# Kernel tuning notes

Hardware: AMD Instinct MI355X
Metric: run time of the kernel (lower is better)

## Reference

```python
import jax, jax.numpy as jnp
from jax import lax
import numpy as np

F_IN, F_OUT, T = 32, 64, 8
H1 = (3 * F_IN + F_OUT) // 4  # 40
H2 = F_OUT                    # 64
N, E = 50000, 800000


def setup_inputs() -> dict:
    key = jax.random.key(0)
    ks = jax.random.split(key, 8)
    def p(k, shape, fan_in):
        return jax.random.normal(k, shape, jnp.float32) / np.float32(np.sqrt(fan_in))
    return {
        "temporal_features": jax.random.normal(ks[0], (N, F_IN, T), jnp.float32),
        "src": jax.random.randint(ks[1], (E,), 0, N, jnp.int32),
        "dst": jax.random.randint(ks[2], (E,), 0, N, jnp.int32),
        "W1": p(ks[3], (F_IN, H1), F_IN), "b1": jnp.zeros((H1,), jnp.float32),
        "W2": p(ks[4], (H1, H2), H1),   "b2": jnp.zeros((H2,), jnp.float32),
        "W3": p(ks[5], (H2, F_OUT), H2), "b3": jnp.zeros((F_OUT,), jnp.float32),
        "Wc": p(ks[6], (F_OUT, F_OUT, 3), F_OUT * 3),  # Conv1d weight [out, in, k]
        "bc": jnp.zeros((F_OUT,), jnp.float32),
    }


def _graph_conv(h, src, dst, out_norm, in_norm, W, b, act, n):
    # dgl GraphConv, norm='both': D_out^{-1/2} -> sum-aggregate -> D_in^{-1/2} -> linear
    h = h * out_norm[:, None, None]                       # [N, t, f]
    agg = jax.ops.segment_sum(h[src], dst, num_segments=n)  # irregular gather/scatter
    h = agg * in_norm[:, None, None]
    h = jnp.einsum("nti,io->nto", h, W) + b
    return jax.nn.relu(h) if act else h


def reference(temporal_features, src, dst, W1, b1, W2, b2, W3, b3, Wc, bc):
    n = temporal_features.shape[0]
    ones = jnp.ones(src.shape, temporal_features.dtype)
    out_deg = jax.ops.segment_sum(ones, src, num_segments=n)
    in_deg = jax.ops.segment_sum(ones, dst, num_segments=n)
    out_norm = jnp.clip(out_deg, 1.0, None) ** -0.5
    in_norm = jnp.clip(in_deg, 1.0, None) ** -0.5

    h = jnp.swapaxes(temporal_features, -2, -1)  # [N, t, f_in]
    h = _graph_conv(h, src, dst, out_norm, in_norm, W1, b1, True, n)
    h = _graph_conv(h, src, dst, out_norm, in_norm, W2, b2, True, n)
    h = _graph_conv(h, src, dst, out_norm, in_norm, W3, b3, False, n)
    h = jnp.swapaxes(h, -2, -1)  # [N, f_out, t]

    out = lax.conv_general_dilated(
        h, Wc, window_strides=(1,), padding=((1, 1),),
        dimension_numbers=("NCH", "OIH", "NCH"))
    return out + bc[None, :, None]
```

## Files before the change

kernel.cpp:

```cpp
#include <hip/hip_runtime.h>

typedef float f32x4 __attribute__((ext_vector_type(4)));


__global__ __launch_bounds__(256) void deg_kernel(const int* __restrict__ src,
                                                  const int* __restrict__ dst,
                                                  int* __restrict__ out_deg,
                                                  int* __restrict__ in_deg, int E) {
  int e = blockIdx.x * 256 + threadIdx.x;
  if (e < E) {
    atomicAdd(&out_deg[src[e]], 1);
    atomicAdd(&in_deg[dst[e]], 1);
  }
}

__global__ __launch_bounds__(256) void norm_kernel(const int* __restrict__ out_deg,
                                                   const int* __restrict__ in_deg,
                                                   float* __restrict__ out_norm,
                                                   float* __restrict__ in_norm, int N) {
  int n = blockIdx.x * 256 + threadIdx.x;
  if (n < N) {
    out_norm[n] = 1.0f / sqrtf((float)max(out_deg[n], 1));
    in_norm[n]  = 1.0f / sqrtf((float)max(in_deg[n], 1));
  }
}

__global__ __launch_bounds__(256) void wct_kernel(const float* __restrict__ Wc,
                                                  float* __restrict__ wct) {
  int m = blockIdx.x * 256 + threadIdx.x;
  if (m < 12288) wct[m] = Wc[(m & 63) * 192 + (m >> 6)];
}


__global__ __launch_bounds__(256) void scan_partial_kernel(const int* __restrict__ deg,
                                                           int* __restrict__ partial, int N) {
  __shared__ int ws[4];
  int tid = threadIdx.x, lane = tid & 63, wv = tid >> 6;
  int base = blockIdx.x * 1024;
  int v = 0;
#pragma unroll
  for (int k = 0; k < 4; ++k) {
    int i = base + tid + k * 256;
    if (i < N) v += deg[i];
  }
  for (int d = 32; d > 0; d >>= 1) v += __shfl_down(v, d, 64);
  if (lane == 0) ws[wv] = v;
  __syncthreads();
  if (tid == 0) partial[blockIdx.x] = ws[0] + ws[1] + ws[2] + ws[3];
}

__global__ __launch_bounds__(1024) void scan_partials_kernel(int* __restrict__ partial, int P) {
  __shared__ int wsum[16];
  int tid = threadIdx.x, lane = tid & 63, wv = tid >> 6;
  int v = (tid < P) ? partial[tid] : 0;
  int x = v;
  for (int d = 1; d < 64; d <<= 1) {
    int y = __shfl_up(x, d, 64);
    if (lane >= d) x += y;
  }
  if (lane == 63) wsum[wv] = x;
  __syncthreads();
  if (wv == 0 && lane < 16) {
    int y = wsum[lane];
    int z = y;
    for (int d = 1; d < 16; d <<= 1) {
      int q = __shfl_up(z, d, 64);
      if (lane >= d) z += q;
    }
    wsum[lane] = z - y;
  }
  __syncthreads();
  if (tid < P) partial[tid] = wsum[wv] + x - v;
}

__global__ __launch_bounds__(1024) void scan_apply_kernel(const int* __restrict__ deg,
                                                          const int* __restrict__ partial,
                                                          int* __restrict__ off, int N) {
  __shared__ int wsum[16];
  int tid = threadIdx.x, lane = tid & 63, wv = tid >> 6;
  int i = blockIdx.x * 1024 + tid;
  int v = (i < N) ? deg[i] : 0;
  int x = v;
  for (int d = 1; d < 64; d <<= 1) {
    int y = __shfl_up(x, d, 64);
    if (lane >= d) x += y;
  }
  if (lane == 63) wsum[wv] = x;
  __syncthreads();
  if (wv == 0 && lane < 16) {
    int y = wsum[lane];
    int z = y;
    for (int d = 1; d < 16; d <<= 1) {
      int q = __shfl_up(z, d, 64);
      if (lane >= d) z += q;
    }
    wsum[lane] = z - y;
  }
  __syncthreads();
  int excl = partial[blockIdx.x] + wsum[wv] + (x - v);
  if (i < N) off[i] = excl;
  if (i == N - 1) off[N] = excl + v;
}

__global__ __launch_bounds__(256) void scatter_kernel(const int* __restrict__ src,
                                                      const int* __restrict__ dst,
                                                      const int* __restrict__ in_off,
                                                      int* __restrict__ cursor,
                                                      int* __restrict__ csr_src, int E) {
  int e = blockIdx.x * 256 + threadIdx.x;
  if (e < E) {
    int d = dst[e];
    int p = atomicAdd(&cursor[d], 1);
    csr_src[in_off[d] + p] = src[e];
  }
}

template <int NC>
__device__ __forceinline__ void keepalive(f32x4* v) {
#pragma unroll
  for (int k = 0; k < NC; ++k) asm volatile("" : "+v"(v[k]));
}

template <int F_IN, int F_OUT, int TS, int L, bool IT_LAYOUT, bool RELU,
          bool GNORM, bool SCALE_OUT>
__device__ __forceinline__ void layer_body(
    const float* __restrict__ h_in, const int* __restrict__ csr_src,
    const int* __restrict__ in_off, const float* __restrict__ out_norm,
    const float* __restrict__ in_norm, const float* __restrict__ W,
    const float* __restrict__ bias, float* __restrict__ h_out, int N) {
  constexpr int NF4 = F_IN * 2;
  constexpr int NC = NF4 / L;
  constexpr int M = 64 / L;
  constexpr int SLOTS = 4 * M;
  constexpr int SLOT = (IT_LAYOUT ? F_IN * 8 : TS * 8) + 8;
  __shared__ float agg[SLOTS][SLOT];
  int tid = threadIdx.x;
  int wave = tid >> 6, lane = tid & 63;
  int q = lane / L, r = lane % L;
  int slot = wave * M + q;
  int n = blockIdx.x * SLOTS + slot;
  bool valid = (n < N);

  f32x4 acc[NC];
#pragma unroll
  for (int k = 0; k < NC; ++k) acc[k] = (f32x4){0.f, 0.f, 0.f, 0.f};

  if (valid) {
    int e0 = in_off[n], e1 = in_off[n + 1];
    const f32x4* h4 = (const f32x4*)h_in;
    int j = e0;
    if (e1 - e0 >= 2) {
      int sA = csr_src[j], sB = csr_src[j + 1];
      do {
        int cA = sA, cB = sB;
        int jn = j + 2;
        sA = csr_src[min(jn, e1 - 1)];
        sB = csr_src[min(jn + 1, e1 - 1)];
        float wA = 1.f, wB = 1.f;
        if constexpr (GNORM) { wA = out_norm[cA]; wB = out_norm[cB]; }
        const f32x4* pA = h4 + (size_t)cA * NF4 + r;
        const f32x4* pB = h4 + (size_t)cB * NF4 + r;
        f32x4 vA[NC], vB[NC];
#pragma unroll
        for (int k = 0; k < NC; ++k) vA[k] = pA[k * L];
#pragma unroll
        for (int k = 0; k < NC; ++k) vB[k] = pB[k * L];
        keepalive<NC>(vA);
        keepalive<NC>(vB);
#pragma unroll
        for (int k = 0; k < NC; ++k)
#pragma unroll
          for (int e = 0; e < 4; ++e) acc[k][e] = fmaf(vA[k][e], wA, acc[k][e]);
#pragma unroll
        for (int k = 0; k < NC; ++k)
#pragma unroll
          for (int e = 0; e < 4; ++e) acc[k][e] = fmaf(vB[k][e], wB, acc[k][e]);
        j = jn;
      } while (j + 2 <= e1);
    }
    if (j < e1) {
      int s = csr_src[j];
      float w = 1.f;
      if constexpr (GNORM) w = out_norm[s];
      const f32x4* p = h4 + (size_t)s * NF4 + r;
#pragma unroll
      for (int k = 0; k < NC; ++k) {
        f32x4 v = p[k * L];
#pragma unroll
        for (int e = 0; e < 4; ++e) acc[k][e] = fmaf(v[e], w, acc[k][e]);
      }
    }
    float innm = in_norm[n];
#pragma unroll
    for (int k = 0; k < NC; ++k) {
      int el = (k * L + r) * 4;
      int addr;
      if constexpr (IT_LAYOUT) {
        addr = el;
      } else {
        int t = el / F_IN;
        int i = el - t * F_IN;
        addr = t * TS + i;
      }
      *(f32x4*)&agg[slot][addr] = acc[k] * innm;
    }
  }

  constexpr int G = F_OUT / 8;
  int t = lane >> 3, og = lane & 7;
  float acc2[M][G];
  {
    float bb[G];
    if constexpr (G == 8) {
      float4 bA = *(const float4*)&bias[og * 8];
      float4 bB = *(const float4*)&bias[og * 8 + 4];
      bb[0] = bA.x; bb[1] = bA.y; bb[2] = bA.z; bb[3] = bA.w;
      bb[4] = bB.x; bb[5] = bB.y; bb[6] = bB.z; bb[7] = bB.w;
    } else {
#pragma unroll
      for (int c = 0; c < G; ++c) bb[c] = bias[og * G + c];
    }
#pragma unroll
    for (int qq = 0; qq < M; ++qq)
#pragma unroll
      for (int c = 0; c < G; ++c) acc2[qq][c] = bb[c];
  }
#pragma unroll 4
  for (int i = 0; i < F_IN; ++i) {
    float wrow[G];
    if constexpr (G == 8) {
      float4 wA = *(const float4*)&W[i * F_OUT + og * 8];
      float4 wB = *(const float4*)&W[i * F_OUT + og * 8 + 4];
      wrow[0] = wA.x; wrow[1] = wA.y; wrow[2] = wA.z; wrow[3] = wA.w;
      wrow[4] = wB.x; wrow[5] = wB.y; wrow[6] = wB.z; wrow[7] = wB.w;
    } else {
#pragma unroll
      for (int c = 0; c < G; ++c) wrow[c] = W[i * F_OUT + og * G + c];
    }
    int raddr;
    if constexpr (IT_LAYOUT) raddr = i * 8 + t;
    else raddr = t * TS + i;
#pragma unroll
    for (int qq = 0; qq < M; ++qq) {
      float a = agg[wave * M + qq][raddr];
#pragma unroll
      for (int c = 0; c < G; ++c) acc2[qq][c] = fmaf(a, wrow[c], acc2[qq][c]);
    }
  }
#pragma unroll
  for (int qq = 0; qq < M; ++qq) {
    int n2 = blockIdx.x * SLOTS + wave * M + qq;
    if (n2 < N) {
      float osc = 1.f;
      if constexpr (SCALE_OUT) osc = out_norm[n2];
      float res[G];
#pragma unroll
      for (int c = 0; c < G; ++c) {
        float v = acc2[qq][c];
        if constexpr (RELU) v = fmaxf(v, 0.f);
        res[c] = v * osc;
      }
      float* orow = h_out + (size_t)n2 * (F_OUT * 8) + t * F_OUT + og * G;
      if constexpr (G == 8) {
        *(float4*)&orow[0] = make_float4(res[0], res[1], res[2], res[3]);
        *(float4*)&orow[4] = make_float4(res[4], res[5], res[6], res[7]);
      } else {
#pragma unroll
        for (int c = 0; c < G; ++c) orow[c] = res[c];
      }
    }
  }
}

__global__ __launch_bounds__(256, 7) void layer1_k(
    const float* __restrict__ h_in, const int* __restrict__ csr_src,
    const int* __restrict__ in_off, const float* __restrict__ out_norm,
    const float* __restrict__ in_norm, const float* __restrict__ W,
    const float* __restrict__ bias, float* __restrict__ h_out, int N) {
  layer_body<32, 40, 0, 16, true, true, true, true>(
      h_in, csr_src, in_off, out_norm, in_norm, W, bias, h_out, N);
}

__global__ __launch_bounds__(256, 6) void layer2_k(
    const float* __restrict__ h_in, const int* __restrict__ csr_src,
    const int* __restrict__ in_off, const float* __restrict__ out_norm,
    const float* __restrict__ in_norm, const float* __restrict__ W,
    const float* __restrict__ bias, float* __restrict__ h_out, int N) {
  layer_body<40, 64, 44, 16, false, true, false, true>(
      h_in, csr_src, in_off, out_norm, in_norm, W, bias, h_out, N);
}

__global__ __launch_bounds__(64, 4) void layer3_conv_k(
    const float* __restrict__ h_in, const int* __restrict__ csr_src,
    const int* __restrict__ in_off, const float* __restrict__ in_norm,
    const float* __restrict__ W, const float* __restrict__ bias,
    const float* __restrict__ wct, const float* __restrict__ bc,
    float* __restrict__ out, int N) {
  constexpr int SLOT = 8 * 68 + 8;
  __shared__ float agg[4][SLOT];
  int lane = threadIdx.x & 63;
  int q = lane >> 4, r = lane & 15;
  int slot = q;
  int n = blockIdx.x * 4 + slot;
  bool valid = (n < N);

  f32x4 acc[8];
#pragma unroll
  for (int k = 0; k < 8; ++k) acc[k] = (f32x4){0.f, 0.f, 0.f, 0.f};

  if (valid) {
    int e0 = in_off[n], e1 = in_off[n + 1];
    const f32x4* h4 = (const f32x4*)h_in;
    int j = e0;
    if (e1 - e0 >= 2) {
      int sA = csr_src[j], sB = csr_src[j + 1];
      do {
        int cA = sA, cB = sB;
        int jn = j + 2;
        sA = csr_src[min(jn, e1 - 1)];
        sB = csr_src[min(jn + 1, e1 - 1)];
        const f32x4* pA = h4 + (size_t)cA * 128 + r;
        const f32x4* pB = h4 + (size_t)cB * 128 + r;
        f32x4 vA[8], vB[8];
#pragma unroll
        for (int k = 0; k < 8; ++k) vA[k] = pA[k * 16];
#pragma unroll
        for (int k = 0; k < 8; ++k) vB[k] = pB[k * 16];
        keepalive<8>(vA);
        keepalive<8>(vB);
#pragma unroll
        for (int k = 0; k < 8; ++k) acc[k] += vA[k];
#pragma unroll
        for (int k = 0; k < 8; ++k) acc[k] += vB[k];
        j = jn;
      } while (j + 2 <= e1);
    }
    if (j < e1) {
      int s = csr_src[j];
      const f32x4* p = h4 + (size_t)s * 128 + r;
#pragma unroll
      for (int k = 0; k < 8; ++k) acc[k] += p[k * 16];
    }
    float innm = in_norm[n];
#pragma unroll
    for (int k = 0; k < 8; ++k) {
      int addr = k * 68 + (r << 2);
      *(f32x4*)&agg[slot][addr] = acc[k] * innm;
    }
  }

  int t = lane >> 3, og = lane & 7;
  float acc2[4][8];
  {
    float4 bA = *(const float4*)&bias[og * 8];
    float4 bB = *(const float4*)&bias[og * 8 + 4];
    float bb[8] = {bA.x, bA.y, bA.z, bA.w, bB.x, bB.y, bB.z, bB.w};
#pragma unroll
    for (int qq = 0; qq < 4; ++qq)
#pragma unroll
      for (int c = 0; c < 8; ++c) acc2[qq][c] = bb[c];
  }
#pragma unroll 4
  for (int i = 0; i < 64; ++i) {
    float4 wA = *(const float4*)&W[i * 64 + og * 8];
    float4 wB = *(const float4*)&W[i * 64 + og * 8 + 4];
    float wrow[8] = {wA.x, wA.y, wA.z, wA.w, wB.x, wB.y, wB.z, wB.w};
    int raddr = t * 68 + i;
#pragma unroll
    for (int qq = 0; qq < 4; ++qq) {
      float a = agg[qq][raddr];
#pragma unroll
      for (int c = 0; c < 8; ++c) acc2[qq][c] = fmaf(a, wrow[c], acc2[qq][c]);
    }
  }

#pragma unroll
  for (int qq = 0; qq < 4; ++qq) {
    float* sb = &agg[qq][og * 64 + t];
#pragma unroll
    for (int c = 0; c < 8; ++c) sb[((c + og) & 7) << 3] = acc2[qq][c];
  }

  float4 b4 = *(const float4*)&bc[r * 4];
  float bcv[4] = {b4.x, b4.y, b4.z, b4.w};
  float cacc[4][8];
#pragma unroll
  for (int c = 0; c < 4; ++c)
#pragma unroll
    for (int tt = 0; tt < 8; ++tt) cacc[c][tt] = bcv[c];

  const float4* wct4 = (const float4*)wct;
  const float* hq = &agg[slot][0];
#pragma unroll 2
  for (int i = 0; i < 64; ++i) {
    int ib = i >> 3, ic = i & 7;
    const float* hi = &hq[ib * 64 + (((ic + ib) & 7) << 3)];
    float4 hA = *(const float4*)hi;
    float4 hB = *(const float4*)(hi + 4);
    float4 w0 = wct4[(i * 3 + 0) * 16 + r];
    float4 w1 = wct4[(i * 3 + 1) * 16 + r];
    float4 w2 = wct4[(i * 3 + 2) * 16 + r];
    float h[8] = {hA.x, hA.y, hA.z, hA.w, hB.x, hB.y, hB.z, hB.w};
    float wk0[4] = {w0.x, w0.y, w0.z, w0.w};
    float wk1[4] = {w1.x, w1.y, w1.z, w1.w};
    float wk2[4] = {w2.x, w2.y, w2.z, w2.w};
#pragma unroll
    for (int c = 0; c < 4; ++c) {
#pragma unroll
      for (int tt = 0; tt < 8; ++tt) cacc[c][tt] = fmaf(wk1[c], h[tt], cacc[c][tt]);
#pragma unroll
      for (int tt = 1; tt < 8; ++tt) cacc[c][tt] = fmaf(wk0[c], h[tt - 1], cacc[c][tt]);
#pragma unroll
      for (int tt = 0; tt < 7; ++tt) cacc[c][tt] = fmaf(wk2[c], h[tt + 1], cacc[c][tt]);
    }
  }
  if (valid) {
    float* ob = out + (size_t)n * 512 + r * 32;
#pragma unroll
    for (int c = 0; c < 4; ++c) {
      *(float4*)&ob[c * 8] = make_float4(cacc[c][0], cacc[c][1], cacc[c][2], cacc[c][3]);
      *(float4*)&ob[c * 8 + 4] = make_float4(cacc[c][4], cacc[c][5], cacc[c][6], cacc[c][7]);
    }
  }
}


extern "C" void kernel_launch(void* const* d_in, const int* in_sizes, int n_in,
                              void* d_out, int out_size, void* d_ws, size_t ws_size,
                              hipStream_t stream) {
  const float* tf = (const float*)d_in[0];
  const int* src = (const int*)d_in[1];
  const int* dst = (const int*)d_in[2];
  const float* W1 = (const float*)d_in[3];
  const float* b1 = (const float*)d_in[4];
  const float* W2 = (const float*)d_in[5];
  const float* b2 = (const float*)d_in[6];
  const float* W3 = (const float*)d_in[7];
  const float* b3 = (const float*)d_in[8];
  const float* Wc = (const float*)d_in[9];
  const float* bc = (const float*)d_in[10];

  int N = in_sizes[0] / 256;
  int E = in_sizes[1];

  char* ws = (char*)d_ws;
  size_t pos = 0;
  auto alloc = [&](size_t bytes) -> void* {
    void* p = ws + pos;
    pos += (bytes + 255) & ~(size_t)255;
    return p;
  };
  int* in_deg   = (int*)alloc((size_t)N * 4);
  int* out_deg  = (int*)alloc((size_t)N * 4);
  int* cursor   = (int*)alloc((size_t)N * 4);
  int* in_off   = (int*)alloc((size_t)(N + 1) * 4);
  int* partial  = (int*)alloc((size_t)1024 * 4);
  float* o_norm = (float*)alloc((size_t)N * 4);
  float* i_norm = (float*)alloc((size_t)N * 4);
  int* csr      = (int*)alloc((size_t)E * 4);
  float* wct    = (float*)alloc((size_t)12288 * 4);
  float* h1     = (float*)alloc((size_t)N * 320 * 4);
  float* h2     = (float*)alloc((size_t)N * 512 * 4);

  hipMemsetAsync(in_deg, 0, (size_t)((char*)in_off - (char*)in_deg), stream);

  deg_kernel<<<(E + 255) / 256, 256, 0, stream>>>(src, dst, out_deg, in_deg, E);
  norm_kernel<<<(N + 255) / 256, 256, 0, stream>>>(out_deg, in_deg, o_norm, i_norm, N);
  wct_kernel<<<48, 256, 0, stream>>>(Wc, wct);

  int P = (N + 1023) / 1024;
  scan_partial_kernel<<<P, 256, 0, stream>>>(in_deg, partial, N);
  scan_partials_kernel<<<1, 1024, 0, stream>>>(partial, P);
  scan_apply_kernel<<<P, 1024, 0, stream>>>(in_deg, partial, in_off, N);

  scatter_kernel<<<(E + 255) / 256, 256, 0, stream>>>(src, dst, in_off, cursor, csr, E);

  layer1_k<<<(N + 15) / 16, 256, 0, stream>>>(tf, csr, in_off, o_norm, i_norm, W1, b1, h1, N);
  layer2_k<<<(N + 15) / 16, 256, 0, stream>>>(h1, csr, in_off, o_norm, i_norm, W2, b2, h2, N);
  layer3_conv_k<<<(N + 3) / 4, 64, 0, stream>>>(h2, csr, in_off, i_norm, W3, b3,
                                                wct, bc, (float*)d_out, N);
}
```

Baseline: 802.1 us.

## Bucket nodes by in-degree and process them in degree-sorted order

Adds a histogram and counting-sort pass that builds a permutation of nodes grouped by in-degree. All three aggregation layers then map each slot to perm[i] rather than to i, so nodes sharing a wave have similar edge counts. The aim is to cut load imbalance and idle lanes in the per-node neighbor gather loops. The cost is three extra small kernels, an indirect node lookup, and scattered rather than sequential output row writes.

```diff
diff --git a/kernel.cpp b/kernel.cpp
--- a/kernel.cpp
+++ b/kernel.cpp
@@ -29,6 +29,25 @@
                                                   float* __restrict__ wct) {
   int m = blockIdx.x * 256 + threadIdx.x;
   if (m < 12288) wct[m] = Wc[(m & 63) * 192 + (m >> 6)];
+}
+
+
+__global__ __launch_bounds__(256) void bhist_kernel(const int* __restrict__ in_deg,
+                                                    int* __restrict__ bh, int N) {
+  int n = blockIdx.x * 256 + threadIdx.x;
+  if (n < N) atomicAdd(&bh[min(in_deg[n], 511)], 1);
+}
+
+__global__ __launch_bounds__(256) void bscatter_kernel(const int* __restrict__ in_deg,
+                                                       const int* __restrict__ bh,
+                                                       int* __restrict__ bcur,
+                                                       int* __restrict__ perm, int N) {
+  int n = blockIdx.x * 256 + threadIdx.x;
+  if (n < N) {
+    int b = min(in_deg[n], 511);
+    int p = atomicAdd(&bcur[b], 1);
+    perm[bh[b] + p] = n;
+  }
 }
 
 
@@ -125,7 +144,8 @@
           bool GNORM, bool SCALE_OUT>
 __device__ __forceinline__ void layer_body(
     const float* __restrict__ h_in, const int* __restrict__ csr_src,
-    const int* __restrict__ in_off, const float* __restrict__ out_norm,
+    const int* __restrict__ in_off, const int* __restrict__ perm,
+    const float* __restrict__ out_norm,
     const float* __restrict__ in_norm, const float* __restrict__ W,
     const float* __restrict__ bias, float* __restrict__ h_out, int N) {
   constexpr int NF4 = F_IN * 2;
@@ -138,8 +158,9 @@
   int wave = tid >> 6, lane = tid & 63;
   int q = lane / L, r = lane % L;
   int slot = wave * M + q;
-  int n = blockIdx.x * SLOTS + slot;
-  bool valid = (n < N);
+  int nl = blockIdx.x * SLOTS + slot;
+  bool valid = (nl < N);
+  int n = valid ? perm[nl] : 0;
 
   f32x4 acc[NC];
 #pragma unroll
@@ -249,8 +270,9 @@
   }
 #pragma unroll
   for (int qq = 0; qq < M; ++qq) {
-    int n2 = blockIdx.x * SLOTS + wave * M + qq;
-    if (n2 < N) {
+    int nl2 = blockIdx.x * SLOTS + wave * M + qq;
+    if (nl2 < N) {
+      int n2 = perm[nl2];
       float osc = 1.f;
       if constexpr (SCALE_OUT) osc = out_norm[n2];
       float res[G];
@@ -274,25 +296,28 @@
 
 __global__ __launch_bounds__(256, 7) void layer1_k(
     const float* __restrict__ h_in, const int* __restrict__ csr_src,
-    const int* __restrict__ in_off, const float* __restrict__ out_norm,
+    const int* __restrict__ in_off, const int* __restrict__ perm,
+    const float* __restrict__ out_norm,
     const float* __restrict__ in_norm, const float* __restrict__ W,
     const float* __restrict__ bias, float* __restrict__ h_out, int N) {
   layer_body<32, 40, 0, 16, true, true, true, true>(
-      h_in, csr_src, in_off, out_norm, in_norm, W, bias, h_out, N);
+      h_in, csr_src, in_off, perm, out_norm, in_norm, W, bias, h_out, N);
 }
 
 __global__ __launch_bounds__(256, 6) void layer2_k(
     const float* __restrict__ h_in, const int* __restrict__ csr_src,
-    const int* __restrict__ in_off, const float* __restrict__ out_norm,
+    const int* __restrict__ in_off, const int* __restrict__ perm,
+    const float* __restrict__ out_norm,
     const float* __restrict__ in_norm, const float* __restrict__ W,
     const float* __restrict__ bias, float* __restrict__ h_out, int N) {
   layer_body<40, 64, 44, 16, false, true, false, true>(
-      h_in, csr_src, in_off, out_norm, in_norm, W, bias, h_out, N);
+      h_in, csr_src, in_off, perm, out_norm, in_norm, W, bias, h_out, N);
 }
 
 __global__ __launch_bounds__(64, 4) void layer3_conv_k(
     const float* __restrict__ h_in, const int* __restrict__ csr_src,
-    const int* __restrict__ in_off, const float* __restrict__ in_norm,
+    const int* __restrict__ in_off, const int* __restrict__ perm,
+    const float* __restrict__ in_norm,
     const float* __restrict__ W, const float* __restrict__ bias,
     const float* __restrict__ wct, const float* __restrict__ bc,
     float* __restrict__ out, int N) {
@@ -301,8 +326,9 @@
   int lane = threadIdx.x & 63;
   int q = lane >> 4, r = lane & 15;
   int slot = q;
-  int n = blockIdx.x * 4 + slot;
-  bool valid = (n < N);
+  int nl = blockIdx.x * 4 + slot;
+  bool valid = (nl < N);
+  int n = valid ? perm[nl] : 0;
 
   f32x4 acc[8];
 #pragma unroll
@@ -453,11 +479,14 @@
   int* in_deg   = (int*)alloc((size_t)N * 4);
   int* out_deg  = (int*)alloc((size_t)N * 4);
   int* cursor   = (int*)alloc((size_t)N * 4);
+  int* bh       = (int*)alloc((size_t)512 * 4);
+  int* bcur     = (int*)alloc((size_t)512 * 4);
   int* in_off   = (int*)alloc((size_t)(N + 1) * 4);
   int* partial  = (int*)alloc((size_t)1024 * 4);
   float* o_norm = (float*)alloc((size_t)N * 4);
   float* i_norm = (float*)alloc((size_t)N * 4);
   int* csr      = (int*)alloc((size_t)E * 4);
+  int* perm     = (int*)alloc((size_t)N * 4);
   float* wct    = (float*)alloc((size_t)12288 * 4);
   float* h1     = (float*)alloc((size_t)N * 320 * 4);
   float* h2     = (float*)alloc((size_t)N * 512 * 4);
@@ -467,6 +496,10 @@
   deg_kernel<<<(E + 255) / 256, 256, 0, stream>>>(src, dst, out_deg, in_deg, E);
   norm_kernel<<<(N + 255) / 256, 256, 0, stream>>>(out_deg, in_deg, o_norm, i_norm, N);
   wct_kernel<<<48, 256, 0, stream>>>(Wc, wct);
+
+  bhist_kernel<<<(N + 255) / 256, 256, 0, stream>>>(in_deg, bh, N);
+  scan_partials_kernel<<<1, 1024, 0, stream>>>(bh, 512);
+  bscatter_kernel<<<(N + 255) / 256, 256, 0, stream>>>(in_deg, bh, bcur, perm, N);
 
   int P = (N + 1023) / 1024;
   scan_partial_kernel<<<P, 256, 0, stream>>>(in_deg, partial, N);
@@ -475,8 +508,10 @@
 
   scatter_kernel<<<(E + 255) / 256, 256, 0, stream>>>(src, dst, in_off, cursor, csr, E);
 
-  layer1_k<<<(N + 15) / 16, 256, 0, stream>>>(tf, csr, in_off, o_norm, i_norm, W1, b1, h1, N);
-  layer2_k<<<(N + 15) / 16, 256, 0, stream>>>(h1, csr, in_off, o_norm, i_norm, W2, b2, h2, N);
-  layer3_conv_k<<<(N + 3) / 4, 64, 0, stream>>>(h2, csr, in_off, i_norm, W3, b3,
+  layer1_k<<<(N + 15) / 16, 256, 0, stream>>>(tf, csr, in_off, perm, o_norm, i_norm,
+                                              W1, b1, h1, N);
+  layer2_k<<<(N + 15) / 16, 256, 0, stream>>>(h1, csr, in_off, perm, o_norm, i_norm,
+                                              W2, b2, h2, N);
+  layer3_conv_k<<<(N + 3) / 4, 64, 0, stream>>>(h2, csr, in_off, perm, i_norm, W3, b3,
                                                 wct, bc, (float*)d_out, N);
 }
```

Result: slower. 1.074 ms (+33.9%).
